# Kernel tuning notes

Measured on AMD Instinct MI355X. Metric: run time of the kernel, lower is better.

## Reference

```python
import jax, jax.numpy as jnp
import numpy as np

B, IN, C, M = 256, 512, 4, 6
S1, S2 = 255, 63          # neurons per layer excluding the prepended bias unit
K = 2 ** M                # contexts per neuron
P = 1e-3                  # pred_clipping
LMIN = float(np.log(P / (1.0 - P)))
LMAX = -LMIN
LR = 1e-3                 # constant learning rate
WCLIP = 5.0               # weight_clipping
BASE_BIAS = 0.0           # fixed base bias logit (original draws uniform in [LMIN, LMAX])


def setup_inputs() -> dict:
    key = jax.random.key(0)
    ks = jax.random.split(key, 10)
    x = jax.random.uniform(ks[0], (B, IN), dtype=jnp.float32)
    target = jax.random.randint(ks[1], (B,), 0, C, dtype=jnp.int32)
    cmaps1 = jax.random.normal(ks[2], (C, S1, M, IN), dtype=jnp.float32)
    w1 = jax.random.uniform(ks[3], (C, S1, K, IN), dtype=jnp.float32) * (2.0 / IN)
    bias1 = jax.random.uniform(ks[4], (1, 1, C), dtype=jnp.float32, minval=LMIN, maxval=LMAX)
    cmaps2 = jax.random.normal(ks[5], (C, S2, M, IN), dtype=jnp.float32)
    w2 = jax.random.uniform(ks[6], (C, S2, K, S1 + 1), dtype=jnp.float32) * (2.0 / (S1 + 1))
    bias2 = jax.random.uniform(ks[7], (1, 1, C), dtype=jnp.float32, minval=LMIN, maxval=LMAX)
    cmaps3 = jax.random.normal(ks[8], (C, 1, M, IN), dtype=jnp.float32)
    w3 = jax.random.uniform(ks[9], (C, 1, K, S2 + 1), dtype=jnp.float32) * (2.0 / (S2 + 1))
    return {"x": x, "target": target, "cmaps1": cmaps1, "w1": w1, "bias1": bias1,
            "cmaps2": cmaps2, "w2": w2, "bias2": bias2, "cmaps3": cmaps3, "w3": w3}


def _layer(logit3, context, tgt, cmaps, weights, bias):
    # logit3: (B, I, Cin) with Cin in {1, C}; context: (B, IN); tgt: (B, C) one-hot
    # cmaps: (C, S, M, IN); weights: (C, S, K, I)
    Cn, S = weights.shape[0], weights.shape[1]
    Bn = context.shape[0]
    # context halfspace gating -> per-(class, neuron, sample) context index
    dist = jnp.einsum('csmk,bk->csmb', cmaps, context)          # (C,S,M,B)
    conv = (2 ** jnp.arange(M, dtype=jnp.int32)).reshape(1, 1, M, 1)
    idx = jnp.sum((dist > 0.0).astype(jnp.int32) * conv, axis=2)  # (C,S,B)
    ci = jnp.arange(Cn)[:, None, None]
    si = jnp.arange(S)[None, :, None]
    sel = weights[ci, si, idx]                                  # gather: (C,S,B,I)
    lg = jnp.broadcast_to(logit3, (Bn, logit3.shape[1], Cn))    # (B,I,C)
    out = jnp.clip(jnp.einsum('csbi,bic->csb', sel, lg), LMIN, LMAX)
    out_t = jnp.transpose(out, (2, 1, 0))                       # (B,S,C)
    # online gradient-style update scattered back into the weight table
    diff = jax.nn.sigmoid(out_t) - tgt[:, None, :]              # (B,S,C)
    upd = LR * diff[..., None] * jnp.transpose(lg, (0, 2, 1))[:, None, :, :]  # (B,S,C,I)
    new_w = weights.at[ci, si, idx].set(
        jnp.clip(sel - jnp.transpose(upd, (2, 1, 0, 3)), -WCLIP, WCLIP))
    if bias is not None:
        out_t = jnp.concatenate([jnp.broadcast_to(bias, (Bn, 1, Cn)), out_t], axis=1)
    return out_t, new_w


def reference(x, target, cmaps1, w1, bias1, cmaps2, w2, bias2, cmaps3, w3):
    tgt = jax.nn.one_hot(target, C, dtype=x.dtype)              # (B,C)
    xb = jnp.clip(x, P, 1.0 - P)
    l0 = jnp.log(xb / (1.0 - xb)).at[:, 0].set(BASE_BIAS)       # base predictions in logit space
    out1, nw1 = _layer(l0[:, :, None], x, tgt, cmaps1, w1, bias1)  # (B,256,C)
    out2, nw2 = _layer(out1, x, tgt, cmaps2, w2, bias2)            # (B,64,C)
    out3, nw3 = _layer(out2, x, tgt, cmaps3, w3, None)             # (B,1,C)
    logits = out3[:, 0, :]                                         # (B,C)
    return (logits, nw1, nw2, nw3)
```

## Files before the change

### kernel.cpp

```cpp
#include <hip/hip_runtime.h>
#include <math.h>

#define B_   256
#define IN_  512
#define C_   4
#define M_   6
#define K_   64
#define S1_  255
#define S2_  63

#define NBLK1 (C_ * S1_)
#define NBLK2 (C_ * S2_)
#define NBLK3 (C_)
#define NBLK_ALL (NBLK1 + NBLK2 + NBLK3)

#define LMIN_ (-6.906754778648554f)
#define LMAX_ ( 6.906754778648554f)
#define LR_   0.001f
#define WCLIP_ 5.0f

__device__ __forceinline__ float clampf(float v, float lo, float hi) {
    return fminf(fmaxf(v, lo), hi);
}

__global__ __launch_bounds__(256) void prep_kernel(const float* __restrict__ x,
                                                   const float* __restrict__ bias1,
                                                   const float* __restrict__ bias2,
                                                   float* __restrict__ xT,
                                                   float* __restrict__ l0,
                                                   float* __restrict__ l0T,
                                                   float* __restrict__ out1T,
                                                   float* __restrict__ out1RM,
                                                   float* __restrict__ out2T,
                                                   float* __restrict__ out2RM) {
    __shared__ float tx_[32][33];
    __shared__ float tl_[32][33];
    const int i0 = (blockIdx.x & 15) * 32;
    const int b0 = (blockIdx.x >> 4) * 32;
    const int tx = threadIdx.x & 31;
    const int ty = threadIdx.x >> 5;
#pragma unroll
    for (int r = 0; r < 4; ++r) {
        int bb = b0 + ty + 8 * r;
        int ii = i0 + tx;
        float xv = x[(size_t)bb * IN_ + ii];
        float xc = clampf(xv, 0.001f, 0.999f);
        float lv = (ii == 0) ? 0.0f : logf(xc / (1.0f - xc));
        l0[(size_t)bb * IN_ + ii] = lv;
        tx_[ty + 8 * r][tx] = xv;
        tl_[ty + 8 * r][tx] = lv;
    }
    __syncthreads();
#pragma unroll
    for (int r = 0; r < 4; ++r) {
        int ii = i0 + ty + 8 * r;
        int bb = b0 + tx;
        xT[(size_t)ii * B_ + bb]  = tx_[tx][ty + 8 * r];
        l0T[(size_t)ii * B_ + bb] = tl_[tx][ty + 8 * r];
    }
    int gid = blockIdx.x * 256 + threadIdx.x;
    if (gid < C_ * B_) {
        int c = gid >> 8, b = gid & 255;
        float b1 = bias1[c], b2 = bias2[c];
        out1T[((size_t)c * (S1_ + 1)) * B_ + b] = b1;
        out1RM[((size_t)c * B_ + b) * (S1_ + 1)] = b1;
        out2T[((size_t)c * (S2_ + 1)) * B_ + b] = b2;
        out2RM[((size_t)c * B_ + b) * (S2_ + 1)] = b2;
    }
}

__global__ __launch_bounds__(256) void route_kernel(
    const float* __restrict__ xT,
    const float* __restrict__ cmaps1,
    const float* __restrict__ cmaps2,
    const float* __restrict__ cmaps3,
    int* __restrict__ idx_buf)
{
    __shared__ float sacc[3][M_][B_];
    const int bid  = blockIdx.x;
    const int wv   = __builtin_amdgcn_readfirstlane(threadIdx.x >> 6);
    const int lane = threadIdx.x & 63;

    const float* cmp;
    if (bid < NBLK1)              cmp = cmaps1 + (size_t)bid * M_ * IN_;
    else if (bid < NBLK1 + NBLK2) cmp = cmaps2 + (size_t)(bid - NBLK1) * M_ * IN_;
    else                          cmp = cmaps3 + (size_t)(bid - NBLK1 - NBLK2) * M_ * IN_;

    float acc[4][M_];
#pragma unroll
    for (int jb = 0; jb < 4; ++jb)
#pragma unroll
        for (int m = 0; m < M_; ++m) acc[jb][m] = 0.0f;

    const int kw = wv * 128;
    for (int k0 = kw; k0 < kw + 128; k0 += 8) {
        float xv[8][4];
#pragma unroll
        for (int j = 0; j < 8; ++j)
#pragma unroll
            for (int jb = 0; jb < 4; ++jb)
                xv[j][jb] = xT[(size_t)(k0 + j) * B_ + 64 * jb + lane];
#pragma unroll
        for (int j = 0; j < 8; ++j)
#pragma unroll
            for (int m = 0; m < M_; ++m) {
                float cv = cmp[(size_t)m * IN_ + k0 + j];
#pragma unroll
                for (int jb = 0; jb < 4; ++jb)
                    acc[jb][m] = fmaf(cv, xv[j][jb], acc[jb][m]);
            }
    }

    if (wv > 0) {
#pragma unroll
        for (int jb = 0; jb < 4; ++jb)
#pragma unroll
            for (int m = 0; m < M_; ++m)
                sacc[wv - 1][m][64 * jb + lane] = acc[jb][m];
    }
    __syncthreads();
    if (wv == 0) {
#pragma unroll
        for (int jb = 0; jb < 4; ++jb) {
            int b = 64 * jb + lane;
            int myidx = 0;
#pragma unroll
            for (int m = 0; m < M_; ++m) {
                float t = acc[jb][m] + sacc[0][m][b] + sacc[1][m][b] + sacc[2][m][b];
                myidx |= (t > 0.0f) ? (1 << m) : 0;
            }
            idx_buf[(size_t)bid * B_ + b] = myidx;
        }
    }
}

template<int DIN, int KSPL>
__global__ __launch_bounds__(256) void dot_kernel(
    const float* __restrict__ lgT, long lgT_sc,
    const float* __restrict__ w,
    const int* __restrict__ idx_buf,
    float* __restrict__ pdot,
    int S)
{
    constexpr int KR  = DIN / KSPL;
    static_assert(KR == 64, "k-slice must be 64");
    constexpr int PAD = 65;
    __shared__ float wl[K_ * PAD];

    const int bid  = blockIdx.x;
    const int tile = bid / KSPL;
    const int ks   = bid % KSPL;
    const int c    = tile / S;
    const int tid  = threadIdx.x;
    const int b    = tid;
    const int k0   = ks * KR;

    const int myrow = idx_buf[(size_t)tile * B_ + b];

    const float* wp = w + (size_t)tile * K_ * DIN + k0;
#pragma unroll
    for (int j = 0; j < 4; ++j) {
        int f   = tid + 256 * j;
        int row = f >> 4;
        int q   = (f & 15) << 2;
        float4 v = *(const float4*)(wp + (size_t)row * DIN + q);
        wl[row * PAD + q + 0] = v.x;
        wl[row * PAD + q + 1] = v.y;
        wl[row * PAD + q + 2] = v.z;
        wl[row * PAD + q + 3] = v.w;
    }
    __syncthreads();

    const float* lgp = lgT + (size_t)c * lgT_sc + (size_t)k0 * B_ + b;
    const float* wr  = wl + myrow * PAD;
    float dot = 0.0f;
    for (int kk = 0; kk < KR; kk += 8) {
        float lv[8];
#pragma unroll
        for (int t = 0; t < 8; ++t) lv[t] = lgp[(size_t)(kk + t) * B_];
#pragma unroll
        for (int t = 0; t < 8; ++t) dot = fmaf(wr[kk + t], lv[t], dot);
    }
    pdot[((size_t)tile * KSPL + ks) * B_ + b] = dot;
}

__global__ __launch_bounds__(256) void fin_kernel(
    const float* __restrict__ pdot, int KSPL,
    const int* __restrict__ idx_buf,
    const int* __restrict__ target,
    float* __restrict__ onextT,
    float* __restrict__ onextRM,
    int* __restrict__ win_g,
    float* __restrict__ dw_g,
    int S, int is_last)
{
    __shared__ float diff_s[B_];
    __shared__ int   win_s[K_];
    const int tile = blockIdx.x;
    const int c    = tile / S;
    const int s    = tile - c * S;
    const int b    = threadIdx.x;

    if (b < K_) win_s[b] = -1;

    float dot = 0.0f;
    for (int j = 0; j < KSPL; ++j)
        dot += pdot[((size_t)tile * KSPL + j) * B_ + b];

    float outv = clampf(dot, LMIN_, LMAX_);
    if (is_last) {
        onextRM[(size_t)b * C_ + c] = outv;
    } else {
        onextT[((size_t)c * (S + 1) + (s + 1)) * B_ + b] = outv;
        onextRM[((size_t)c * B_ + b) * (size_t)(S + 1) + (s + 1)] = outv;
    }
    float tg = (target[b] == c) ? 1.0f : 0.0f;
    diff_s[b] = 1.0f / (1.0f + expf(-outv)) - tg;
    const int myrow = idx_buf[(size_t)tile * B_ + b];
    __syncthreads();
    atomicMax(&win_s[myrow], b);
    __syncthreads();
    if (b < K_) {
        int bw = win_s[b];
        win_g[(size_t)tile * K_ + b] = bw;
        dw_g[(size_t)tile * K_ + b]  = (bw >= 0) ? LR_ * diff_s[bw] : 0.0f;
    }
}

template<int DIN>
__global__ __launch_bounds__(256) void update_kernel(
    const float* __restrict__ w,
    const float* __restrict__ lgRM, long lg_sc,
    const int* __restrict__ win_g,
    const float* __restrict__ dw_g,
    float* __restrict__ nw,
    int SK)
{
    constexpr int QPR = DIN / 4;
    constexpr int QSH = (DIN == 512) ? 7 : (DIN == 256) ? 6 : 4;
    const int base = blockIdx.x * 2048 + threadIdx.x;
#pragma unroll
    for (int j = 0; j < 8; ++j) {
        int Q   = base + j * 256;
        int row = Q >> QSH;
        int col = (Q & (QPR - 1)) << 2;
        float4 wv = *(const float4*)(w + (size_t)row * DIN + col);
        int bw = win_g[row];
        if (bw >= 0) {
            float d = dw_g[row];
            int cc  = row / SK;
            const float4 lv = *(const float4*)(lgRM + (size_t)cc * lg_sc + (size_t)bw * DIN + col);
            wv.x = clampf(wv.x - d * lv.x, -WCLIP_, WCLIP_);
            wv.y = clampf(wv.y - d * lv.y, -WCLIP_, WCLIP_);
            wv.z = clampf(wv.z - d * lv.z, -WCLIP_, WCLIP_);
            wv.w = clampf(wv.w - d * lv.w, -WCLIP_, WCLIP_);
        }
        *(float4*)(nw + (size_t)row * DIN + col) = wv;
    }
}

extern "C" void kernel_launch(void* const* d_in, const int* in_sizes, int n_in,
                              void* d_out, int out_size, void* d_ws, size_t ws_size,
                              hipStream_t stream) {
    const float* x      = (const float*)d_in[0];
    const int*   target = (const int*)  d_in[1];
    const float* cmaps1 = (const float*)d_in[2];
    const float* w1     = (const float*)d_in[3];
    const float* bias1  = (const float*)d_in[4];
    const float* cmaps2 = (const float*)d_in[5];
    const float* w2     = (const float*)d_in[6];
    const float* bias2  = (const float*)d_in[7];
    const float* cmaps3 = (const float*)d_in[8];
    const float* w3     = (const float*)d_in[9];
    float* out = (float*)d_out;

    float* xT      = (float*)d_ws;
    float* l0      = xT     + (size_t)IN_ * B_;
    float* l0T     = l0     + (size_t)B_ * IN_;
    float* out1T   = l0T    + (size_t)IN_ * B_;
    float* out1RM  = out1T  + (size_t)C_ * (S1_ + 1) * B_;
    float* out2T   = out1RM + (size_t)C_ * B_ * (S1_ + 1);
    float* out2RM  = out2T  + (size_t)C_ * (S2_ + 1) * B_;
    float* pdot    = out2RM + (size_t)C_ * B_ * (S2_ + 1);
    float* dw_g    = pdot   + (size_t)NBLK1 * 8 * B_;
    int*   win_g   = (int*)(dw_g + (size_t)NBLK_ALL * K_);
    int*   idx_buf = (int*)(win_g + (size_t)NBLK_ALL * K_);

    float* logits = out;
    float* nw1 = out + (size_t)B_ * C_;
    float* nw2 = nw1 + (size_t)C_ * S1_ * K_ * IN_;
    float* nw3 = nw2 + (size_t)C_ * S2_ * K_ * (S1_ + 1);

    prep_kernel<<<dim3(128), dim3(256), 0, stream>>>(
        x, bias1, bias2, xT, l0, l0T, out1T, out1RM, out2T, out2RM);

    route_kernel<<<dim3(NBLK_ALL), dim3(256), 0, stream>>>(
        xT, cmaps1, cmaps2, cmaps3, idx_buf);

    const int* idx1 = idx_buf;
    const int* idx2 = idx_buf + (size_t)NBLK1 * B_;
    const int* idx3 = idx_buf + (size_t)(NBLK1 + NBLK2) * B_;
    int*   win1 = win_g;                         float* dw1 = dw_g;
    int*   win2 = win_g + NBLK1 * K_;            float* dw2 = dw_g + NBLK1 * K_;
    int*   win3 = win_g + (NBLK1 + NBLK2) * K_;  float* dw3 = dw_g + (NBLK1 + NBLK2) * K_;

    dot_kernel<512, 8><<<dim3(NBLK1 * 8), dim3(256), 0, stream>>>(
        l0T, 0L, w1, idx1, pdot, S1_);
    fin_kernel<<<dim3(NBLK1), dim3(256), 0, stream>>>(
        pdot, 8, idx1, target, out1T, out1RM, win1, dw1, S1_, 0);
    update_kernel<512><<<dim3(NBLK1 * K_ * 128 / 2048), dim3(256), 0, stream>>>(
        w1, l0, 0L, win1, dw1, nw1, S1_ * K_);

    dot_kernel<256, 4><<<dim3(NBLK2 * 4), dim3(256), 0, stream>>>(
        out1T, (long)(S1_ + 1) * B_, w2, idx2, pdot, S2_);
    fin_kernel<<<dim3(NBLK2), dim3(256), 0, stream>>>(
        pdot, 4, idx2, target, out2T, out2RM, win2, dw2, S2_, 0);
    update_kernel<256><<<dim3(NBLK2 * K_ * 64 / 2048), dim3(256), 0, stream>>>(
        w2, out1RM, (long)B_ * (S1_ + 1), win2, dw2, nw2, S2_ * K_);

    dot_kernel<64, 1><<<dim3(NBLK3), dim3(256), 0, stream>>>(
        out2T, (long)(S2_ + 1) * B_, w3, idx3, pdot, 1);
    fin_kernel<<<dim3(NBLK3), dim3(256), 0, stream>>>(
        pdot, 1, idx3, target, nullptr, logits, win3, dw3, 1, 1);
    update_kernel<64><<<dim3(NBLK3 * K_ * 16 / 2048), dim3(256), 0, stream>>>(
        w3, out2RM, (long)B_ * (S2_ + 1), win3, dw3, nw3, K_);
}
```

Measured before the change: 154.5 us.

## Fuse finalize and weight-update kernels, recomputing winners per update block

The separate finalize and update kernels are merged into one launch per layer. The first ntiles blocks write the layer outputs, and the remaining blocks each recompute the dot sum, sigmoid diff and last-writer winners in shared memory before updating a slice of the weight table. This removes the win/dw global buffers and one launch per layer. The cost is redundant recomputation of the winner selection in every update sub-block. Weight-table output writes now use nontemporal stores.

Result: faster. 140.2 us (-9.3%).

```diff
diff --git a/kernel.cpp b/kernel.cpp
--- a/kernel.cpp
+++ b/kernel.cpp
@@ -18,6 +18,8 @@
 #define LMAX_ ( 6.906754778648554f)
 #define LR_   0.001f
 #define WCLIP_ 5.0f
+
+typedef float v4f __attribute__((ext_vector_type(4)));
 
 __device__ __forceinline__ float clampf(float v, float lo, float hi) {
     return fminf(fmaxf(v, lo), hi);
@@ -184,78 +186,94 @@
     pdot[((size_t)tile * KSPL + ks) * B_ + b] = dot;
 }
 
-__global__ __launch_bounds__(256) void fin_kernel(
-    const float* __restrict__ pdot, int KSPL,
+template<int DIN, int KSPL, int UPB>
+__global__ __launch_bounds__(256) void finup_kernel(
+    const float* __restrict__ pdot,
     const int* __restrict__ idx_buf,
     const int* __restrict__ target,
+    const float* __restrict__ lgRM, long lg_sc,
+    const float* __restrict__ w,
+    float* __restrict__ nw,
     float* __restrict__ onextT,
     float* __restrict__ onextRM,
-    int* __restrict__ win_g,
-    float* __restrict__ dw_g,
-    int S, int is_last)
+    int S, int ntiles, int is_last)
 {
+    constexpr int ROWS = K_ / UPB;
+    constexpr int QPR  = DIN / 4;
+    constexpr int QSH  = (DIN == 512) ? 7 : (DIN == 256) ? 6 : 4;
+    constexpr int ITER = ROWS * QPR / 256;
+
     __shared__ float diff_s[B_];
+    __shared__ float dw_s[K_];
     __shared__ int   win_s[K_];
-    const int tile = blockIdx.x;
+
+    const int bid = blockIdx.x;
+    const int tid = threadIdx.x;
+    const int b   = tid;
+
+    if (bid < ntiles) {
+        const int tile = bid;
+        const int c    = tile / S;
+        const int s    = tile - c * S;
+        float dot = 0.0f;
+#pragma unroll
+        for (int j = 0; j < KSPL; ++j)
+            dot += pdot[((size_t)tile * KSPL + j) * B_ + b];
+        float outv = clampf(dot, LMIN_, LMAX_);
+        if (is_last) {
+            onextRM[(size_t)b * C_ + c] = outv;
+        } else {
+            onextT[((size_t)c * (S + 1) + (s + 1)) * B_ + b] = outv;
+            onextRM[((size_t)c * B_ + b) * (size_t)(S + 1) + (s + 1)] = outv;
+        }
+        return;
+    }
+
+    const int ub   = bid - ntiles;
+    const int tile = ub / UPB;
+    const int sub  = ub - tile * UPB;
     const int c    = tile / S;
-    const int s    = tile - c * S;
-    const int b    = threadIdx.x;
-
-    if (b < K_) win_s[b] = -1;
+
+    if (tid < K_) win_s[tid] = -1;
 
     float dot = 0.0f;
+#pragma unroll
     for (int j = 0; j < KSPL; ++j)
         dot += pdot[((size_t)tile * KSPL + j) * B_ + b];
-
     float outv = clampf(dot, LMIN_, LMAX_);
-    if (is_last) {
-        onextRM[(size_t)b * C_ + c] = outv;
-    } else {
-        onextT[((size_t)c * (S + 1) + (s + 1)) * B_ + b] = outv;
-        onextRM[((size_t)c * B_ + b) * (size_t)(S + 1) + (s + 1)] = outv;
-    }
     float tg = (target[b] == c) ? 1.0f : 0.0f;
     diff_s[b] = 1.0f / (1.0f + expf(-outv)) - tg;
     const int myrow = idx_buf[(size_t)tile * B_ + b];
     __syncthreads();
     atomicMax(&win_s[myrow], b);
     __syncthreads();
-    if (b < K_) {
-        int bw = win_s[b];
-        win_g[(size_t)tile * K_ + b] = bw;
-        dw_g[(size_t)tile * K_ + b]  = (bw >= 0) ? LR_ * diff_s[bw] : 0.0f;
-    }
-}
-
-template<int DIN>
-__global__ __launch_bounds__(256) void update_kernel(
-    const float* __restrict__ w,
-    const float* __restrict__ lgRM, long lg_sc,
-    const int* __restrict__ win_g,
-    const float* __restrict__ dw_g,
-    float* __restrict__ nw,
-    int SK)
-{
-    constexpr int QPR = DIN / 4;
-    constexpr int QSH = (DIN == 512) ? 7 : (DIN == 256) ? 6 : 4;
-    const int base = blockIdx.x * 2048 + threadIdx.x;
-#pragma unroll
-    for (int j = 0; j < 8; ++j) {
-        int Q   = base + j * 256;
+    if (tid < K_) {
+        int bw = win_s[tid];
+        dw_s[tid] = (bw >= 0) ? LR_ * diff_s[bw] : 0.0f;
+    }
+    __syncthreads();
+
+    const int r0 = sub * ROWS;
+    const float* wp  = w  + ((size_t)tile * K_ + r0) * DIN;
+    float*       nwp = nw + ((size_t)tile * K_ + r0) * DIN;
+    const float* lgc = lgRM + (size_t)c * lg_sc;
+#pragma unroll
+    for (int j = 0; j < ITER; ++j) {
+        int Q   = tid + 256 * j;
         int row = Q >> QSH;
         int col = (Q & (QPR - 1)) << 2;
-        float4 wv = *(const float4*)(w + (size_t)row * DIN + col);
-        int bw = win_g[row];
+        float4 wv = *(const float4*)(wp + (size_t)row * DIN + col);
+        int bw = win_s[r0 + row];
         if (bw >= 0) {
-            float d = dw_g[row];
-            int cc  = row / SK;
-            const float4 lv = *(const float4*)(lgRM + (size_t)cc * lg_sc + (size_t)bw * DIN + col);
+            float d = dw_s[r0 + row];
+            const float4 lv = *(const float4*)(lgc + (size_t)bw * DIN + col);
             wv.x = clampf(wv.x - d * lv.x, -WCLIP_, WCLIP_);
             wv.y = clampf(wv.y - d * lv.y, -WCLIP_, WCLIP_);
             wv.z = clampf(wv.z - d * lv.z, -WCLIP_, WCLIP_);
             wv.w = clampf(wv.w - d * lv.w, -WCLIP_, WCLIP_);
         }
-        *(float4*)(nw + (size_t)row * DIN + col) = wv;
+        v4f o = {wv.x, wv.y, wv.z, wv.w};
+        __builtin_nontemporal_store(o, (v4f*)(nwp + (size_t)row * DIN + col));
     }
 }
 
@@ -282,9 +300,7 @@
     float* out2T   = out1RM + (size_t)C_ * B_ * (S1_ + 1);
     float* out2RM  = out2T  + (size_t)C_ * (S2_ + 1) * B_;
     float* pdot    = out2RM + (size_t)C_ * B_ * (S2_ + 1);
-    float* dw_g    = pdot   + (size_t)NBLK1 * 8 * B_;
-    int*   win_g   = (int*)(dw_g + (size_t)NBLK_ALL * K_);
-    int*   idx_buf = (int*)(win_g + (size_t)NBLK_ALL * K_);
+    int*   idx_buf = (int*)(pdot + (size_t)NBLK1 * 8 * B_);
 
     float* logits = out;
     float* nw1 = out + (size_t)B_ * C_;
@@ -300,28 +316,19 @@
     const int* idx1 = idx_buf;
     const int* idx2 = idx_buf + (size_t)NBLK1 * B_;
     const int* idx3 = idx_buf + (size_t)(NBLK1 + NBLK2) * B_;
-    int*   win1 = win_g;                         float* dw1 = dw_g;
-    int*   win2 = win_g + NBLK1 * K_;            float* dw2 = dw_g + NBLK1 * K_;
-    int*   win3 = win_g + (NBLK1 + NBLK2) * K_;  float* dw3 = dw_g + (NBLK1 + NBLK2) * K_;
 
     dot_kernel<512, 8><<<dim3(NBLK1 * 8), dim3(256), 0, stream>>>(
         l0T, 0L, w1, idx1, pdot, S1_);
-    fin_kernel<<<dim3(NBLK1), dim3(256), 0, stream>>>(
-        pdot, 8, idx1, target, out1T, out1RM, win1, dw1, S1_, 0);
-    update_kernel<512><<<dim3(NBLK1 * K_ * 128 / 2048), dim3(256), 0, stream>>>(
-        w1, l0, 0L, win1, dw1, nw1, S1_ * K_);
+    finup_kernel<512, 8, 4><<<dim3(NBLK1 * 5), dim3(256), 0, stream>>>(
+        pdot, idx1, target, l0, 0L, w1, nw1, out1T, out1RM, S1_, NBLK1, 0);
 
     dot_kernel<256, 4><<<dim3(NBLK2 * 4), dim3(256), 0, stream>>>(
         out1T, (long)(S1_ + 1) * B_, w2, idx2, pdot, S2_);
-    fin_kernel<<<dim3(NBLK2), dim3(256), 0, stream>>>(
-        pdot, 4, idx2, target, out2T, out2RM, win2, dw2, S2_, 0);
-    update_kernel<256><<<dim3(NBLK2 * K_ * 64 / 2048), dim3(256), 0, stream>>>(
-        w2, out1RM, (long)B_ * (S1_ + 1), win2, dw2, nw2, S2_ * K_);
+    finup_kernel<256, 4, 2><<<dim3(NBLK2 * 3), dim3(256), 0, stream>>>(
+        pdot, idx2, target, out1RM, (long)B_ * (S1_ + 1), w2, nw2, out2T, out2RM, S2_, NBLK2, 0);
 
     dot_kernel<64, 1><<<dim3(NBLK3), dim3(256), 0, stream>>>(
         out2T, (long)(S2_ + 1) * B_, w3, idx3, pdot, 1);
-    fin_kernel<<<dim3(NBLK3), dim3(256), 0, stream>>>(
-        pdot, 1, idx3, target, nullptr, logits, win3, dw3, 1, 1);
-    update_kernel<64><<<dim3(NBLK3 * K_ * 16 / 2048), dim3(256), 0, stream>>>(
-        w3, out2RM, (long)B_ * (S2_ + 1), win3, dw3, nw3, K_);
-}
+    finup_kernel<64, 1, 1><<<dim3(NBLK3 * 2), dim3(256), 0, stream>>>(
+        pdot, idx3, target, out2RM, (long)B_ * (S2_ + 1), w3, nw3, nullptr, logits, 1, NBLK3, 1);
+}
```

## Overlap layer weight updates with next-layer dot products and fuse final stage

Applied to the files above, without the earlier changes.

Each layer's weight-table update now runs in the same launch as the next layer's gated dot product, using a mixed kernel that splits blocks by index. The last layer's finalize and update are merged into one kernel. The routing kernel handles two neurons per block to reuse the loaded x values. Weight-table writes use nontemporal stores. The aim is to cut launch count and idle tail time between the small dependent kernels and to hide the bandwidth-heavy update behind the dot work, at the cost of higher register use in routing and a mixed-shape grid.

Result: faster. 138.2 us (-10.6%).

```diff
diff --git a/kernel.cpp b/kernel.cpp
--- a/kernel.cpp
+++ b/kernel.cpp
@@ -18,6 +18,8 @@
 #define LMAX_ ( 6.906754778648554f)
 #define LR_   0.001f
 #define WCLIP_ 5.0f
+
+typedef float v4f __attribute__((ext_vector_type(4)));
 
 __device__ __forceinline__ float clampf(float v, float lo, float hi) {
     return fminf(fmaxf(v, lo), hi);
@@ -76,21 +78,27 @@
     const float* __restrict__ cmaps3,
     int* __restrict__ idx_buf)
 {
-    __shared__ float sacc[3][M_][B_];
-    const int bid  = blockIdx.x;
+    __shared__ float sacc[3][2][M_][B_];
     const int wv   = __builtin_amdgcn_readfirstlane(threadIdx.x >> 6);
     const int lane = threadIdx.x & 63;
-
-    const float* cmp;
-    if (bid < NBLK1)              cmp = cmaps1 + (size_t)bid * M_ * IN_;
-    else if (bid < NBLK1 + NBLK2) cmp = cmaps2 + (size_t)(bid - NBLK1) * M_ * IN_;
-    else                          cmp = cmaps3 + (size_t)(bid - NBLK1 - NBLK2) * M_ * IN_;
-
-    float acc[4][M_];
-#pragma unroll
-    for (int jb = 0; jb < 4; ++jb)
-#pragma unroll
-        for (int m = 0; m < M_; ++m) acc[jb][m] = 0.0f;
+    const int t0   = blockIdx.x * 2;
+
+    const float* cmp[2];
+#pragma unroll
+    for (int u = 0; u < 2; ++u) {
+        int bid = t0 + u;
+        if (bid < NBLK1)              cmp[u] = cmaps1 + (size_t)bid * M_ * IN_;
+        else if (bid < NBLK1 + NBLK2) cmp[u] = cmaps2 + (size_t)(bid - NBLK1) * M_ * IN_;
+        else                          cmp[u] = cmaps3 + (size_t)(bid - NBLK1 - NBLK2) * M_ * IN_;
+    }
+
+    float acc[2][4][M_];
+#pragma unroll
+    for (int u = 0; u < 2; ++u)
+#pragma unroll
+        for (int jb = 0; jb < 4; ++jb)
+#pragma unroll
+            for (int m = 0; m < M_; ++m) acc[u][jb][m] = 0.0f;
 
     const int kw = wv * 128;
     for (int k0 = kw; k0 < kw + 128; k0 += 8) {
@@ -103,51 +111,57 @@
 #pragma unroll
         for (int j = 0; j < 8; ++j)
 #pragma unroll
-            for (int m = 0; m < M_; ++m) {
-                float cv = cmp[(size_t)m * IN_ + k0 + j];
-#pragma unroll
-                for (int jb = 0; jb < 4; ++jb)
-                    acc[jb][m] = fmaf(cv, xv[j][jb], acc[jb][m]);
+            for (int u = 0; u < 2; ++u)
+#pragma unroll
+                for (int m = 0; m < M_; ++m) {
+                    float cv = cmp[u][(size_t)m * IN_ + k0 + j];
+#pragma unroll
+                    for (int jb = 0; jb < 4; ++jb)
+                        acc[u][jb][m] = fmaf(cv, xv[j][jb], acc[u][jb][m]);
+                }
+    }
+
+    if (wv > 0) {
+#pragma unroll
+        for (int u = 0; u < 2; ++u)
+#pragma unroll
+            for (int jb = 0; jb < 4; ++jb)
+#pragma unroll
+                for (int m = 0; m < M_; ++m)
+                    sacc[wv - 1][u][m][64 * jb + lane] = acc[u][jb][m];
+    }
+    __syncthreads();
+    if (wv == 0) {
+#pragma unroll
+        for (int u = 0; u < 2; ++u)
+#pragma unroll
+            for (int jb = 0; jb < 4; ++jb) {
+                int b = 64 * jb + lane;
+                int myidx = 0;
+#pragma unroll
+                for (int m = 0; m < M_; ++m) {
+                    float t = acc[u][jb][m] + sacc[0][u][m][b] + sacc[1][u][m][b] + sacc[2][u][m][b];
+                    myidx |= (t > 0.0f) ? (1 << m) : 0;
+                }
+                idx_buf[(size_t)(t0 + u) * B_ + b] = myidx;
             }
     }
-
-    if (wv > 0) {
-#pragma unroll
-        for (int jb = 0; jb < 4; ++jb)
-#pragma unroll
-            for (int m = 0; m < M_; ++m)
-                sacc[wv - 1][m][64 * jb + lane] = acc[jb][m];
-    }
-    __syncthreads();
-    if (wv == 0) {
-#pragma unroll
-        for (int jb = 0; jb < 4; ++jb) {
-            int b = 64 * jb + lane;
-            int myidx = 0;
-#pragma unroll
-            for (int m = 0; m < M_; ++m) {
-                float t = acc[jb][m] + sacc[0][m][b] + sacc[1][m][b] + sacc[2][m][b];
-                myidx |= (t > 0.0f) ? (1 << m) : 0;
-            }
-            idx_buf[(size_t)bid * B_ + b] = myidx;
-        }
-    }
-}
+}
+
 
 template<int DIN, int KSPL>
-__global__ __launch_bounds__(256) void dot_kernel(
+__device__ __forceinline__ void dot_body(
+    int bid,
     const float* __restrict__ lgT, long lgT_sc,
     const float* __restrict__ w,
     const int* __restrict__ idx_buf,
     float* __restrict__ pdot,
-    int S)
+    int S, float* wl)
 {
     constexpr int KR  = DIN / KSPL;
     static_assert(KR == 64, "k-slice must be 64");
     constexpr int PAD = 65;
-    __shared__ float wl[K_ * PAD];
-
-    const int bid  = blockIdx.x;
+
     const int tile = bid / KSPL;
     const int ks   = bid % KSPL;
     const int c    = tile / S;
@@ -184,51 +198,9 @@
     pdot[((size_t)tile * KSPL + ks) * B_ + b] = dot;
 }
 
-__global__ __launch_bounds__(256) void fin_kernel(
-    const float* __restrict__ pdot, int KSPL,
-    const int* __restrict__ idx_buf,
-    const int* __restrict__ target,
-    float* __restrict__ onextT,
-    float* __restrict__ onextRM,
-    int* __restrict__ win_g,
-    float* __restrict__ dw_g,
-    int S, int is_last)
-{
-    __shared__ float diff_s[B_];
-    __shared__ int   win_s[K_];
-    const int tile = blockIdx.x;
-    const int c    = tile / S;
-    const int s    = tile - c * S;
-    const int b    = threadIdx.x;
-
-    if (b < K_) win_s[b] = -1;
-
-    float dot = 0.0f;
-    for (int j = 0; j < KSPL; ++j)
-        dot += pdot[((size_t)tile * KSPL + j) * B_ + b];
-
-    float outv = clampf(dot, LMIN_, LMAX_);
-    if (is_last) {
-        onextRM[(size_t)b * C_ + c] = outv;
-    } else {
-        onextT[((size_t)c * (S + 1) + (s + 1)) * B_ + b] = outv;
-        onextRM[((size_t)c * B_ + b) * (size_t)(S + 1) + (s + 1)] = outv;
-    }
-    float tg = (target[b] == c) ? 1.0f : 0.0f;
-    diff_s[b] = 1.0f / (1.0f + expf(-outv)) - tg;
-    const int myrow = idx_buf[(size_t)tile * B_ + b];
-    __syncthreads();
-    atomicMax(&win_s[myrow], b);
-    __syncthreads();
-    if (b < K_) {
-        int bw = win_s[b];
-        win_g[(size_t)tile * K_ + b] = bw;
-        dw_g[(size_t)tile * K_ + b]  = (bw >= 0) ? LR_ * diff_s[bw] : 0.0f;
-    }
-}
-
 template<int DIN>
-__global__ __launch_bounds__(256) void update_kernel(
+__device__ __forceinline__ void update_body(
+    int ub,
     const float* __restrict__ w,
     const float* __restrict__ lgRM, long lg_sc,
     const int* __restrict__ win_g,
@@ -238,7 +210,7 @@
 {
     constexpr int QPR = DIN / 4;
     constexpr int QSH = (DIN == 512) ? 7 : (DIN == 256) ? 6 : 4;
-    const int base = blockIdx.x * 2048 + threadIdx.x;
+    const int base = ub * 2048 + threadIdx.x;
 #pragma unroll
     for (int j = 0; j < 8; ++j) {
         int Q   = base + j * 256;
@@ -255,7 +227,132 @@
             wv.z = clampf(wv.z - d * lv.z, -WCLIP_, WCLIP_);
             wv.w = clampf(wv.w - d * lv.w, -WCLIP_, WCLIP_);
         }
-        *(float4*)(nw + (size_t)row * DIN + col) = wv;
+        v4f o = {wv.x, wv.y, wv.z, wv.w};
+        __builtin_nontemporal_store(o, (v4f*)(nw + (size_t)row * DIN + col));
+    }
+}
+
+template<int DIN, int KSPL>
+__global__ __launch_bounds__(256) void dot_kernel(
+    const float* __restrict__ lgT, long lgT_sc,
+    const float* __restrict__ w,
+    const int* __restrict__ idx_buf,
+    float* __restrict__ pdot, int S)
+{
+    __shared__ float wl[K_ * 65];
+    dot_body<DIN, KSPL>(blockIdx.x, lgT, lgT_sc, w, idx_buf, pdot, S, wl);
+}
+
+__global__ __launch_bounds__(256) void fin_kernel(
+    const float* __restrict__ pdot, int KSPL,
+    const int* __restrict__ idx_buf,
+    const int* __restrict__ target,
+    float* __restrict__ onextT,
+    float* __restrict__ onextRM,
+    int* __restrict__ win_g,
+    float* __restrict__ dw_g,
+    int S)
+{
+    __shared__ float diff_s[B_];
+    __shared__ int   win_s[K_];
+    const int tile = blockIdx.x;
+    const int c    = tile / S;
+    const int s    = tile - c * S;
+    const int b    = threadIdx.x;
+
+    if (b < K_) win_s[b] = -1;
+
+    float dot = 0.0f;
+    for (int j = 0; j < KSPL; ++j)
+        dot += pdot[((size_t)tile * KSPL + j) * B_ + b];
+
+    float outv = clampf(dot, LMIN_, LMAX_);
+    onextT[((size_t)c * (S + 1) + (s + 1)) * B_ + b] = outv;
+    onextRM[((size_t)c * B_ + b) * (size_t)(S + 1) + (s + 1)] = outv;
+
+    float tg = (target[b] == c) ? 1.0f : 0.0f;
+    diff_s[b] = 1.0f / (1.0f + expf(-outv)) - tg;
+    const int myrow = idx_buf[(size_t)tile * B_ + b];
+    __syncthreads();
+    atomicMax(&win_s[myrow], b);
+    __syncthreads();
+    if (b < K_) {
+        int bw = win_s[b];
+        win_g[(size_t)tile * K_ + b] = bw;
+        dw_g[(size_t)tile * K_ + b]  = (bw >= 0) ? LR_ * diff_s[bw] : 0.0f;
+    }
+}
+
+template<int DIN_D, int KSPL_D, int DIN_U>
+__global__ __launch_bounds__(256) void mix_kernel(
+    const float* __restrict__ lgT, long lgT_sc,
+    const float* __restrict__ wD,
+    const int* __restrict__ idxD,
+    float* __restrict__ pdot, int SD, int ndot,
+    const float* __restrict__ wU,
+    const float* __restrict__ lgRM, long lg_sc,
+    const int* __restrict__ win_g,
+    const float* __restrict__ dw_g,
+    float* __restrict__ nwU, int SKU)
+{
+    __shared__ float wl[K_ * 65];
+    if ((int)blockIdx.x < ndot)
+        dot_body<DIN_D, KSPL_D>(blockIdx.x, lgT, lgT_sc, wD, idxD, pdot, SD, wl);
+    else
+        update_body<DIN_U>(blockIdx.x - ndot, wU, lgRM, lg_sc, win_g, dw_g, nwU, SKU);
+}
+
+__global__ __launch_bounds__(256) void fin3u_kernel(
+    const float* __restrict__ pdot,
+    const int* __restrict__ idx3,
+    const int* __restrict__ target,
+    const float* __restrict__ lgRM, long lg_sc,
+    const float* __restrict__ w3,
+    float* __restrict__ nw3,
+    float* __restrict__ logits)
+{
+    __shared__ float diff_s[B_];
+    __shared__ float dw_s[K_];
+    __shared__ int   win_s[K_];
+    const int c = blockIdx.x;
+    const int b = threadIdx.x;
+
+    if (b < K_) win_s[b] = -1;
+
+    float outv = clampf(pdot[(size_t)c * B_ + b], LMIN_, LMAX_);
+    logits[(size_t)b * C_ + c] = outv;
+    float tg = (target[b] == c) ? 1.0f : 0.0f;
+    diff_s[b] = 1.0f / (1.0f + expf(-outv)) - tg;
+    const int myrow = idx3[(size_t)c * B_ + b];
+    __syncthreads();
+    atomicMax(&win_s[myrow], b);
+    __syncthreads();
+    if (b < K_) {
+        int bw = win_s[b];
+        dw_s[b] = (bw >= 0) ? LR_ * diff_s[bw] : 0.0f;
+    }
+    __syncthreads();
+
+    const float* lgc = lgRM + (size_t)c * lg_sc;
+    const float* wp  = w3  + (size_t)c * K_ * 64;
+    float*       nwp = nw3 + (size_t)c * K_ * 64;
+#pragma unroll
+    for (int j = 0; j < 4; ++j) {
+        int Q   = b + 256 * j;
+        int row = Q >> 4;
+        int col = (Q & 15) << 2;
+        float4 wv = *(const float4*)(wp + row * 64 + col);
+        int bw = win_s[row];
+        if (bw >= 0) {
+            float d = dw_s[row];
+            const float4 lv = *(const float4*)(lgc + (size_t)bw * 64 + col);
+            wv.x = clampf(wv.x - d * lv.x, -WCLIP_, WCLIP_);
+            wv.y = clampf(wv.y - d * lv.y, -WCLIP_, WCLIP_);
+            wv.z = clampf(wv.z - d * lv.z, -WCLIP_, WCLIP_);
+            wv.w = clampf(wv.w - d * lv.w, -WCLIP_, WCLIP_);
+        }
+        v4f o = {wv.x, wv.y, wv.z, wv.w};
+        __builtin_nontemporal_store(o, (v4f*)(nwp + row * 64 + col));
     }
 }
 
@@ -291,37 +388,33 @@
     float* nw2 = nw1 + (size_t)C_ * S1_ * K_ * IN_;
     float* nw3 = nw2 + (size_t)C_ * S2_ * K_ * (S1_ + 1);
 
-    prep_kernel<<<dim3(128), dim3(256), 0, stream>>>(
-        x, bias1, bias2, xT, l0, l0T, out1T, out1RM, out2T, out2RM);
-
-    route_kernel<<<dim3(NBLK_ALL), dim3(256), 0, stream>>>(
-        xT, cmaps1, cmaps2, cmaps3, idx_buf);
-
     const int* idx1 = idx_buf;
     const int* idx2 = idx_buf + (size_t)NBLK1 * B_;
     const int* idx3 = idx_buf + (size_t)(NBLK1 + NBLK2) * B_;
     int*   win1 = win_g;                         float* dw1 = dw_g;
     int*   win2 = win_g + NBLK1 * K_;            float* dw2 = dw_g + NBLK1 * K_;
-    int*   win3 = win_g + (NBLK1 + NBLK2) * K_;  float* dw3 = dw_g + (NBLK1 + NBLK2) * K_;
+
+    prep_kernel<<<dim3(128), dim3(256), 0, stream>>>(
+        x, bias1, bias2, xT, l0, l0T, out1T, out1RM, out2T, out2RM);
+
+    route_kernel<<<dim3(NBLK_ALL / 2), dim3(256), 0, stream>>>(
+        xT, cmaps1, cmaps2, cmaps3, idx_buf);
 
     dot_kernel<512, 8><<<dim3(NBLK1 * 8), dim3(256), 0, stream>>>(
         l0T, 0L, w1, idx1, pdot, S1_);
     fin_kernel<<<dim3(NBLK1), dim3(256), 0, stream>>>(
-        pdot, 8, idx1, target, out1T, out1RM, win1, dw1, S1_, 0);
-    update_kernel<512><<<dim3(NBLK1 * K_ * 128 / 2048), dim3(256), 0, stream>>>(
+        pdot, 8, idx1, target, out1T, out1RM, win1, dw1, S1_);
+
+    mix_kernel<256, 4, 512><<<dim3(NBLK2 * 4 + NBLK1 * 4), dim3(256), 0, stream>>>(
+        out1T, (long)(S1_ + 1) * B_, w2, idx2, pdot, S2_, NBLK2 * 4,
         w1, l0, 0L, win1, dw1, nw1, S1_ * K_);
-
-    dot_kernel<256, 4><<<dim3(NBLK2 * 4), dim3(256), 0, stream>>>(
-        out1T, (long)(S1_ + 1) * B_, w2, idx2, pdot, S2_);
     fin_kernel<<<dim3(NBLK2), dim3(256), 0, stream>>>(
-        pdot, 4, idx2, target, out2T, out2RM, win2, dw2, S2_, 0);
-    update_kernel<256><<<dim3(NBLK2 * K_ * 64 / 2048), dim3(256), 0, stream>>>(
+        pdot, 4, idx2, target, out2T, out2RM, win2, dw2, S2_);
+
+    mix_kernel<64, 1, 256><<<dim3(NBLK3 + NBLK2 * 2), dim3(256), 0, stream>>>(
+        out2T, (long)(S2_ + 1) * B_, w3, idx3, pdot, 1, NBLK3,
         w2, out1RM, (long)B_ * (S1_ + 1), win2, dw2, nw2, S2_ * K_);
 
-    dot_kernel<64, 1><<<dim3(NBLK3), dim3(256), 0, stream>>>(
-        out2T, (long)(S2_ + 1) * B_, w3, idx3, pdot, 1);
-    fin_kernel<<<dim3(NBLK3), dim3(256), 0, stream>>>(
-        pdot, 1, idx3, target, nullptr, logits, win3, dw3, 1, 1);
-    update_kernel<64><<<dim3(NBLK3 * K_ * 16 / 2048), dim3(256), 0, stream>>>(
-        w3, out2RM, (long)B_ * (S2_ + 1), win3, dw3, nw3, K_);
-}
+    fin3u_kernel<<<dim3(NBLK3), dim3(256), 0, stream>>>(
+        pdot, idx3, target, out2RM, (long)B_ * (S2_ + 1), w3, nw3, logits);
+}
```
